# Optimization experiments

Measured on AMD Instinct MI355X. Metric: run time of the kernel, lower is better.

Reference implementation:

```python
import jax, jax.numpy as jnp
import numpy as np

N, E, G = 50000, 800000, 64        # nodes, edges, graphs in batch
IN, HID, OUT = 64, 128, 8


def gcn_conv(x, W, b, src, dst, num_nodes):
    """GCNConv: h = D^-1/2 (A+I) D^-1/2 (x W) + b, self-loops already in src/dst."""
    h = x @ W                                              # [N, out]
    deg = jax.ops.segment_sum(jnp.ones_like(dst, dtype=h.dtype), dst,
                              num_segments=num_nodes)      # [N]
    dinv = jax.lax.rsqrt(jnp.maximum(deg, 1.0))
    norm = dinv[src] * dinv[dst]                           # [E+N]
    msg = h[src] * norm[:, None]                           # gather + scale
    out = jax.ops.segment_sum(msg, dst, num_segments=num_nodes)
    return out + b


def global_mean_pool(x, batch, num_graphs):
    s = jax.ops.segment_sum(x, batch, num_segments=num_graphs)
    cnt = jax.ops.segment_sum(jnp.ones((x.shape[0],), x.dtype), batch,
                              num_segments=num_graphs)
    return s / jnp.maximum(cnt, 1.0)[:, None]


def setup_inputs() -> dict:
    key = jax.random.key(0)
    ks = jax.random.split(key, 11)
    def glorot(k, fi, fo):
        return jax.random.normal(k, (fi, fo), jnp.float32) * np.float32(1.0 / np.sqrt(fi))
    return {
        "x": jax.random.normal(ks[0], (N, IN), jnp.float32),
        "W1": glorot(ks[1], IN, HID),  "b1": jnp.zeros((HID,), jnp.float32),
        "W2": glorot(ks[2], HID, HID), "b2": jnp.zeros((HID,), jnp.float32),
        "W3": glorot(ks[3], HID, HID), "b3": jnp.zeros((HID,), jnp.float32),
        "Wh": glorot(ks[4], HID, OUT), "bh": jnp.zeros((OUT,), jnp.float32),
        "edge_index": jax.random.randint(ks[5], (2, E), 0, N),
        "batch": jnp.sort(jax.random.randint(ks[6], (N,), 0, G)),
    }


def reference(x, W1, b1, W2, b2, W3, b3, Wh, bh, edge_index, batch):
    loops = jnp.arange(N, dtype=edge_index.dtype)
    src = jnp.concatenate([edge_index[0], loops])          # add self-loops
    dst = jnp.concatenate([edge_index[1], loops])
    h = jax.nn.relu(gcn_conv(x, W1, b1, src, dst, N))
    h = jax.nn.relu(gcn_conv(h, W2, b2, src, dst, N))
    h = gcn_conv(h, W3, b3, src, dst, N)
    g = global_mean_pool(h, batch, G)                      # [G, HID]
    return g @ Wh + bh                                     # [G, OUT]
```

## Files before the change

### kernel.cpp

```cpp
#include <hip/hip_runtime.h>

typedef short bf8_t __attribute__((ext_vector_type(8)));
typedef float f32x4 __attribute__((ext_vector_type(4)));
typedef unsigned short u16;

__device__ inline u16 f2bf(float f) {
    unsigned u = __float_as_uint(f);
    return (u16)((u + 0x7fff + ((u >> 16) & 1)) >> 16);
}


__global__ void deg_kernel(const int* __restrict__ dst, int* __restrict__ deg,
                           u16* __restrict__ rank, int E) {
    int e = blockIdx.x * 256 + threadIdx.x;
    if (e < E) rank[e] = (u16)atomicAdd(&deg[dst[e]], 1);
}

__global__ void scan_blocksum(const int* __restrict__ deg, int* __restrict__ bsum,
                              float* __restrict__ dinv, int n) {
    int i = blockIdx.x * 256 + threadIdx.x;
    int d = (i < n) ? (deg[i] + 1) : 0;
    if (i < n) dinv[i] = rsqrtf((float)d);
    int v = d;
    for (int off = 32; off > 0; off >>= 1) v += __shfl_down(v, off, 64);
    __shared__ int ws[4];
    if ((threadIdx.x & 63) == 0) ws[threadIdx.x >> 6] = v;
    __syncthreads();
    if (threadIdx.x == 0) bsum[blockIdx.x] = ws[0] + ws[1] + ws[2] + ws[3];
}

__global__ void scan_offsets(const int* __restrict__ bsum, int* __restrict__ boff, int nblk) {
    __shared__ int buf[256];
    int tid = threadIdx.x;
    int v = (tid < nblk) ? bsum[tid] : 0;
    buf[tid] = v;
    __syncthreads();
    for (int off = 1; off < 256; off <<= 1) {
        int t = (tid >= off) ? buf[tid - off] : 0;
        __syncthreads();
        buf[tid] += t;
        __syncthreads();
    }
    if (tid < nblk) boff[tid] = buf[tid] - v;
}

__global__ void scan_rowptr(const int* __restrict__ deg, const int* __restrict__ boff,
                            int* __restrict__ row_ptr, int n) {
    __shared__ int buf[256];
    int tid = threadIdx.x;
    int i = blockIdx.x * 256 + tid;
    int v = (i < n) ? (deg[i] + 1) : 0;
    buf[tid] = v;
    __syncthreads();
    for (int off = 1; off < 256; off <<= 1) {
        int t = (tid >= off) ? buf[tid - off] : 0;
        __syncthreads();
        buf[tid] += t;
        __syncthreads();
    }
    int excl = buf[tid] - v + boff[blockIdx.x];
    if (i < n) row_ptr[i] = excl;
    if (i == n - 1) row_ptr[n] = excl + v;
}

__global__ void fill_kernel(const int* __restrict__ src, const int* __restrict__ dst,
                            const u16* __restrict__ rank,
                            const int* __restrict__ row_ptr,
                            u16* __restrict__ csr_src, int E, int n) {
    int e = blockIdx.x * 256 + threadIdx.x;
    if (e < E) {
        int s = src[e], d = dst[e];
        int pos = row_ptr[d] + 1 + (int)rank[e];
        __builtin_nontemporal_store((u16)s, &csr_src[pos]);
    } else if (e < E + n) {
        int s = e - E;
        __builtin_nontemporal_store((u16)s, &csr_src[row_ptr[s]]);
    }
}

__global__ void x2bf_kernel(const float* __restrict__ x, const float* __restrict__ dinv,
                            unsigned* __restrict__ x16, int total8) {
    int i = blockIdx.x * 256 + threadIdx.x;
    if (i >= total8) return;
    float dn = dinv[i >> 3];
    const float4* x4 = (const float4*)x;
    float4 a = x4[i * 2], b = x4[i * 2 + 1];
    uint4 o;
    o.x = (unsigned)f2bf(a.x * dn) | ((unsigned)f2bf(a.y * dn) << 16);
    o.y = (unsigned)f2bf(a.z * dn) | ((unsigned)f2bf(a.w * dn) << 16);
    o.z = (unsigned)f2bf(b.x * dn) | ((unsigned)f2bf(b.y * dn) << 16);
    o.w = (unsigned)f2bf(b.z * dn) | ((unsigned)f2bf(b.w * dn) << 16);
    ((uint4*)x16)[i] = o;
}

__global__ void wt_all(const float* __restrict__ W1, const float* __restrict__ W2,
                       const float* __restrict__ W3,
                       u16* __restrict__ Wt1, u16* __restrict__ Wt2,
                       u16* __restrict__ Wt3) {
    int i = blockIdx.x * 256 + threadIdx.x;
    if (i < 8192) {
        int nn = i / 64, k = i - nn * 64;
        Wt1[i] = f2bf(W1[k * 128 + nn]);
    } else if (i < 24576) {
        int j = i - 8192;
        int nn = j / 128, k = j - nn * 128;
        Wt2[j] = f2bf(W2[k * 128 + nn]);
    } else if (i < 40960) {
        int j = i - 24576;
        int nn = j / 128, k = j - nn * 128;
        Wt3[j] = f2bf(W3[k * 128 + nn]);
    }
}


__device__ inline void bf8_add(uint4 a, float* acc) {
#pragma unroll
    for (int j = 0; j < 4; ++j) {
        unsigned u = ((const unsigned*)&a)[j];
        acc[2 * j]     += __uint_as_float(u << 16);
        acc[2 * j + 1] += __uint_as_float(u & 0xffff0000u);
    }
}

__device__ inline uint4 pack_bf8(const float* v, float dn) {
    uint4 o;
    o.x = (unsigned)f2bf(v[0] * dn) | ((unsigned)f2bf(v[1] * dn) << 16);
    o.y = (unsigned)f2bf(v[2] * dn) | ((unsigned)f2bf(v[3] * dn) << 16);
    o.z = (unsigned)f2bf(v[4] * dn) | ((unsigned)f2bf(v[5] * dn) << 16);
    o.w = (unsigned)f2bf(v[6] * dn) | ((unsigned)f2bf(v[7] * dn) << 16);
    return o;
}

template<int K, bool RELU, bool BF16OUT>
__global__ __launch_bounds__(256) void agg_gemm(
        const u16* __restrict__ in, const u16* __restrict__ Wt16,
        const float* __restrict__ bias, void* __restrict__ outp,
        const int* __restrict__ row_ptr, const u16* __restrict__ csr_src,
        const float* __restrict__ dinv, int n) {
    constexpr int KS = K / 32;
    __shared__ u16 As[16 * K];
    int w = threadIdx.x >> 6, lane = threadIdx.x & 63;
    int base = blockIdx.x * 16;
    int lr = lane & 15, lk = lane >> 4;

    bf8_t B[2][KS];
#pragma unroll
    for (int f = 0; f < 2; ++f) {
        int col = w * 32 + f * 16 + lr;
#pragma unroll
        for (int ks = 0; ks < KS; ++ks)
            B[f][ks] = *reinterpret_cast<const bf8_t*>(&Wt16[(size_t)col * K + ks * 32 + lk * 8]);
    }

    const uint4* in4 = (const uint4*)in;
    int g = lane >> 4;
    int row = w * 4 + g;
    int node = base + row;
    float acc[8] = {0.f, 0.f, 0.f, 0.f, 0.f, 0.f, 0.f, 0.f};

    if (K == 128) {
        int col = lane & 15;
        if (node < n) {
            int beg = row_ptr[node], end = row_ptr[node + 1];
            int i = beg;
            int s0 = csr_src[i], s1 = csr_src[i + 1];
            for (; i + 1 < end; i += 2) {
                int t0 = csr_src[i + 2], t1 = csr_src[i + 3];
                uint4 a = in4[(size_t)s0 * 16 + col];
                uint4 b = in4[(size_t)s1 * 16 + col];
                bf8_add(a, acc);
                bf8_add(b, acc);
                s0 = t0; s1 = t1;
            }
            if (i < end) bf8_add(in4[(size_t)s0 * 16 + col], acc);
        }
        float dn = (node < n) ? dinv[node] : 0.f;
        int off = row * K + ((col * 8) ^ ((row & 7) << 3));
        *(uint4*)&As[off] = pack_bf8(acc, dn);
    } else {
        int sub = (lane >> 3) & 1;
        int col = lane & 7;
        if (node < n) {
            int beg = row_ptr[node], end = row_ptr[node + 1];
            int i = beg + sub;
            int s0 = csr_src[i], s1 = csr_src[i + 2];
            for (; i + 2 < end; i += 4) {
                int t0 = csr_src[i + 4], t1 = csr_src[i + 6];
                uint4 a = in4[(size_t)s0 * 8 + col];
                uint4 b = in4[(size_t)s1 * 8 + col];
                bf8_add(a, acc);
                bf8_add(b, acc);
                s0 = t0; s1 = t1;
            }
            if (i < end) bf8_add(in4[(size_t)s0 * 8 + col], acc);
        }
#pragma unroll
        for (int j = 0; j < 8; ++j)
            acc[j] += __shfl_xor(acc[j], 8, 64);
        if (sub == 0) {
            float dn = (node < n) ? dinv[node] : 0.f;
            int off = row * K + ((col * 8) ^ ((row & 7) << 3));
            *(uint4*)&As[off] = pack_bf8(acc, dn);
        }
    }
    __syncthreads();

    f32x4 pacc[2] = {};
#pragma unroll
    for (int ks = 0; ks < KS; ++ks) {
        int off = lr * K + (((ks * 32) + lk * 8) ^ ((lr & 7) << 3));
        bf8_t a = *reinterpret_cast<const bf8_t*>(&As[off]);
#pragma unroll
        for (int f = 0; f < 2; ++f)
            pacc[f] = __builtin_amdgcn_mfma_f32_16x16x32_bf16(B[f][ks], a, pacc[f], 0, 0, 0);
    }

    int orow = base + lr;
    if (orow < n) {
        float dnx = BF16OUT ? dinv[orow] : 1.f;
#pragma unroll
        for (int f = 0; f < 2; ++f) {
            int c0 = w * 32 + f * 16 + lk * 4;
            float4 bv = *(const float4*)&bias[c0];
            float v0 = pacc[f][0] + bv.x, v1 = pacc[f][1] + bv.y;
            float v2 = pacc[f][2] + bv.z, v3 = pacc[f][3] + bv.w;
            if (RELU) {
                v0 = fmaxf(v0, 0.f); v1 = fmaxf(v1, 0.f);
                v2 = fmaxf(v2, 0.f); v3 = fmaxf(v3, 0.f);
            }
            if (BF16OUT) {
                uint2 o;
                o.x = (unsigned)f2bf(v0 * dnx) | ((unsigned)f2bf(v1 * dnx) << 16);
                o.y = (unsigned)f2bf(v2 * dnx) | ((unsigned)f2bf(v3 * dnx) << 16);
                *(uint2*)&((u16*)outp)[(size_t)orow * 128 + c0] = o;
            } else {
                *(float4*)&((float*)outp)[(size_t)orow * 128 + c0] = make_float4(v0, v1, v2, v3);
            }
        }
    }
}


__device__ inline int lbound(const int* __restrict__ batch, int n, int g) {
    int lo = 0, hi = n;
    while (lo < hi) {
        int mid = (lo + hi) >> 1;
        if (batch[mid] < g) lo = mid + 1; else hi = mid;
    }
    return lo;
}

#define PSPLIT 16
__global__ __launch_bounds__(256) void pool_part(
        const float* __restrict__ h, const int* __restrict__ batch,
        float* __restrict__ part, int n) {
    int g = blockIdx.x >> 4, sp = blockIdx.x & (PSPLIT - 1);
    int tid = threadIdx.x;
    int c = tid & 127, rs = tid >> 7;
    int beg = lbound(batch, n, g), end = lbound(batch, n, g + 1);
    int len = end - beg;
    int chunk = (len + PSPLIT - 1) >> 4;
    int r0 = beg + sp * chunk;
    int r1 = min(r0 + chunk, end);
    float acc = 0.f;
    for (int r = r0 + rs; r < r1; r += 2)
        acc += h[(size_t)r * 128 + c];
    __shared__ float buf[256];
    buf[tid] = acc;
    __syncthreads();
    if (rs == 0)
        part[(size_t)blockIdx.x * 128 + c] = buf[c] + buf[c + 128];
}

__global__ __launch_bounds__(128) void pool_final(
        const float* __restrict__ part, const int* __restrict__ batch,
        float* __restrict__ gout, int n) {
    int g = blockIdx.x;
    int c = threadIdx.x;
    float acc = 0.f;
#pragma unroll
    for (int sp = 0; sp < PSPLIT; ++sp)
        acc += part[((size_t)g * PSPLIT + sp) * 128 + c];
    int cnt = lbound(batch, n, g + 1) - lbound(batch, n, g);
    gout[g * 128 + c] = acc / fmaxf((float)cnt, 1.f);
}

__global__ void head_kernel(const float* __restrict__ g, const float* __restrict__ Wh,
                            const float* __restrict__ bh, float* __restrict__ out, int G) {
    int tid = blockIdx.x * blockDim.x + threadIdx.x;
    if (tid >= G * 8) return;
    int gi = tid >> 3, o = tid & 7;
    float acc = bh[o];
    for (int k = 0; k < 128; ++k)
        acc = fmaf(g[gi * 128 + k], Wh[k * 8 + o], acc);
    out[tid] = acc;
}


extern "C" void kernel_launch(void* const* d_in, const int* in_sizes, int n_in,
                              void* d_out, int out_size, void* d_ws, size_t ws_size,
                              hipStream_t stream) {
    const float* x  = (const float*)d_in[0];
    const float* W1 = (const float*)d_in[1];
    const float* b1 = (const float*)d_in[2];
    const float* W2 = (const float*)d_in[3];
    const float* b2 = (const float*)d_in[4];
    const float* W3 = (const float*)d_in[5];
    const float* b3 = (const float*)d_in[6];
    const float* Wh = (const float*)d_in[7];
    const float* bh = (const float*)d_in[8];
    const int* edge_index = (const int*)d_in[9];
    const int* batch = (const int*)d_in[10];
    (void)n_in; (void)ws_size;

    const int N = in_sizes[10];
    const int E = in_sizes[9] / 2;
    const int G = out_size / 8;
    const int* esrc = edge_index;
    const int* edst = edge_index + E;

    size_t off = 0;
    auto take = [&](size_t bytes) {
        void* p = (char*)d_ws + off;
        off += (bytes + 255) & ~(size_t)255;
        return p;
    };
    int*   deg      = (int*)take((size_t)N * 4);
    float* dinv     = (float*)take((size_t)N * 4);
    int*   row_ptr  = (int*)take((size_t)(N + 1) * 4);
    u16*   rank     = (u16*)take((size_t)E * 2);
    u16*   csr_src  = (u16*)take((size_t)(E + N + 64) * 2);
    int*   bsum     = (int*)take(256 * 4);
    int*   boff     = (int*)take(256 * 4);
    float* part     = (float*)take((size_t)G * PSPLIT * 128 * 4);
    float* gpool    = (float*)take((size_t)G * 128 * 4);
    u16*   x16      = (u16*)take((size_t)N * 64 * 2);
    u16*   h16a     = (u16*)take((size_t)N * 128 * 2);
    u16*   h16b     = (u16*)take((size_t)N * 128 * 2);
    u16*   Wt1      = (u16*)take((size_t)128 * 64 * 2);
    u16*   Wt2      = (u16*)take((size_t)128 * 128 * 2);
    u16*   Wt3      = (u16*)take((size_t)128 * 128 * 2);
    float* bufA     = (float*)take((size_t)N * 128 * 4);

    int nblk = (N + 255) / 256;
    int fgrid = (N + 15) / 16;

    hipMemsetAsync(deg, 0, (size_t)N * 4, stream);

    deg_kernel<<<(E + 255) / 256, 256, 0, stream>>>(edst, deg, rank, E);
    scan_blocksum<<<nblk, 256, 0, stream>>>(deg, bsum, dinv, N);
    scan_offsets<<<1, 256, 0, stream>>>(bsum, boff, nblk);
    scan_rowptr<<<nblk, 256, 0, stream>>>(deg, boff, row_ptr, N);
    fill_kernel<<<(E + N + 255) / 256, 256, 0, stream>>>(esrc, edst, rank, row_ptr, csr_src, E, N);
    x2bf_kernel<<<(N * 64 / 8 + 255) / 256, 256, 0, stream>>>(x, dinv, (unsigned*)x16, N * 64 / 8);
    wt_all<<<(40960 + 255) / 256, 256, 0, stream>>>(W1, W2, W3, Wt1, Wt2, Wt3);

    agg_gemm<64,  true,  true ><<<fgrid, 256, 0, stream>>>(x16,  Wt1, b1, h16a, row_ptr, csr_src, dinv, N);
    agg_gemm<128, true,  true ><<<fgrid, 256, 0, stream>>>(h16a, Wt2, b2, h16b, row_ptr, csr_src, dinv, N);
    agg_gemm<128, false, false><<<fgrid, 256, 0, stream>>>(h16b, Wt3, b3, bufA, row_ptr, csr_src, dinv, N);

    pool_part<<<G * PSPLIT, 256, 0, stream>>>(bufA, batch, part, N);
    pool_final<<<G, 128, 0, stream>>>(part, batch, gpool, N);
    head_kernel<<<(G * 8 + 255) / 256, 256, 0, stream>>>(gpool, Wh, bh, (float*)d_out, G);
}
```

Baseline: 224.5 us.

## Fuse prep kernels and pooling head; use nontemporal gather loads

Merges the CSR fill, x-to-bf16 conversion and weight transpose kernels into one prep launch, and folds the head matmul into the pool-final kernel, so there are fewer kernel launches and gaps between them. The neighbour-feature gathers in the aggregation kernels now use nontemporal loads through a vector type. The intent is to cut launch overhead and to reduce cache pollution from the random gathers. The risk is that nontemporal hints hurt reuse, because feature rows are gathered many times and could otherwise be served from L2.

```diff
diff --git a/kernel.cpp b/kernel.cpp
--- a/kernel.cpp
+++ b/kernel.cpp
@@ -2,6 +2,7 @@
 
 typedef short bf8_t __attribute__((ext_vector_type(8)));
 typedef float f32x4 __attribute__((ext_vector_type(4)));
+typedef unsigned u32x4 __attribute__((ext_vector_type(4)));
 typedef unsigned short u16;
 
 __device__ inline u16 f2bf(float f) {
@@ -63,71 +64,73 @@
     if (i == n - 1) row_ptr[n] = excl + v;
 }
 
-__global__ void fill_kernel(const int* __restrict__ src, const int* __restrict__ dst,
-                            const u16* __restrict__ rank,
-                            const int* __restrict__ row_ptr,
-                            u16* __restrict__ csr_src, int E, int n) {
-    int e = blockIdx.x * 256 + threadIdx.x;
-    if (e < E) {
-        int s = src[e], d = dst[e];
-        int pos = row_ptr[d] + 1 + (int)rank[e];
+
+__global__ void prep_kernel(const int* __restrict__ src, const int* __restrict__ dst,
+                            const u16* __restrict__ rank, const int* __restrict__ row_ptr,
+                            u16* __restrict__ csr_src,
+                            const float* __restrict__ x, const float* __restrict__ dinv,
+                            unsigned* __restrict__ x16,
+                            const float* __restrict__ W1, const float* __restrict__ W2,
+                            const float* __restrict__ W3,
+                            u16* __restrict__ Wt1, u16* __restrict__ Wt2,
+                            u16* __restrict__ Wt3,
+                            int E, int n, int total8) {
+    int gid = blockIdx.x * 256 + threadIdx.x;
+    if (gid < E) {
+        int s = src[gid], d = dst[gid];
+        int pos = row_ptr[d] + 1 + (int)rank[gid];
         __builtin_nontemporal_store((u16)s, &csr_src[pos]);
-    } else if (e < E + n) {
-        int s = e - E;
+        return;
+    }
+    if (gid < E + n) {
+        int s = gid - E;
         __builtin_nontemporal_store((u16)s, &csr_src[row_ptr[s]]);
-    }
-}
-
-__global__ void x2bf_kernel(const float* __restrict__ x, const float* __restrict__ dinv,
-                            unsigned* __restrict__ x16, int total8) {
-    int i = blockIdx.x * 256 + threadIdx.x;
-    if (i >= total8) return;
-    float dn = dinv[i >> 3];
-    const float4* x4 = (const float4*)x;
-    float4 a = x4[i * 2], b = x4[i * 2 + 1];
-    uint4 o;
-    o.x = (unsigned)f2bf(a.x * dn) | ((unsigned)f2bf(a.y * dn) << 16);
-    o.y = (unsigned)f2bf(a.z * dn) | ((unsigned)f2bf(a.w * dn) << 16);
-    o.z = (unsigned)f2bf(b.x * dn) | ((unsigned)f2bf(b.y * dn) << 16);
-    o.w = (unsigned)f2bf(b.z * dn) | ((unsigned)f2bf(b.w * dn) << 16);
-    ((uint4*)x16)[i] = o;
-}
-
-__global__ void wt_all(const float* __restrict__ W1, const float* __restrict__ W2,
-                       const float* __restrict__ W3,
-                       u16* __restrict__ Wt1, u16* __restrict__ Wt2,
-                       u16* __restrict__ Wt3) {
-    int i = blockIdx.x * 256 + threadIdx.x;
-    if (i < 8192) {
-        int nn = i / 64, k = i - nn * 64;
-        Wt1[i] = f2bf(W1[k * 128 + nn]);
-    } else if (i < 24576) {
-        int j = i - 8192;
-        int nn = j / 128, k = j - nn * 128;
-        Wt2[j] = f2bf(W2[k * 128 + nn]);
-    } else if (i < 40960) {
-        int j = i - 24576;
-        int nn = j / 128, k = j - nn * 128;
-        Wt3[j] = f2bf(W3[k * 128 + nn]);
-    }
-}
-
-
-__device__ inline void bf8_add(uint4 a, float* acc) {
+        return;
+    }
+    int i = gid - (E + n);
+    if (i < total8) {
+        float dn = dinv[i >> 3];
+        const float4* x4 = (const float4*)x;
+        float4 a = x4[i * 2], b = x4[i * 2 + 1];
+        uint4 o;
+        o.x = (unsigned)f2bf(a.x * dn) | ((unsigned)f2bf(a.y * dn) << 16);
+        o.y = (unsigned)f2bf(a.z * dn) | ((unsigned)f2bf(a.w * dn) << 16);
+        o.z = (unsigned)f2bf(b.x * dn) | ((unsigned)f2bf(b.y * dn) << 16);
+        o.w = (unsigned)f2bf(b.z * dn) | ((unsigned)f2bf(b.w * dn) << 16);
+        ((uint4*)x16)[i] = o;
+        return;
+    }
+    int j = i - total8;
+    if (j < 8192) {
+        int nn = j / 64, k = j - nn * 64;
+        Wt1[j] = f2bf(W1[k * 128 + nn]);
+    } else if (j < 24576) {
+        int jj = j - 8192;
+        int nn = jj / 128, k = jj - nn * 128;
+        Wt2[jj] = f2bf(W2[k * 128 + nn]);
+    } else if (j < 40960) {
+        int jj = j - 24576;
+        int nn = jj / 128, k = jj - nn * 128;
+        Wt3[jj] = f2bf(W3[k * 128 + nn]);
+    }
+}
+
+
+__device__ inline void bf8_add(u32x4 a, float* acc) {
 #pragma unroll
     for (int j = 0; j < 4; ++j) {
-        unsigned u = ((const unsigned*)&a)[j];
+        unsigned u = a[j];
         acc[2 * j]     += __uint_as_float(u << 16);
         acc[2 * j + 1] += __uint_as_float(u & 0xffff0000u);
     }
 }
 
-__device__ inline uint4 pack_bf8(const float* v, float dn) {
-    uint4 o;
-    o.x = (unsigned)f2bf(v[0] * dn) | ((unsigned)f2bf(v[1] * dn) << 16);
-    o.y = (unsigned)f2bf(v[2] * dn) | ((unsigned)f2bf(v[3] * dn) << 16);
-    o.z = (unsigned)f2bf(v[4] * dn) | ((unsigned)f2bf(v[5] * dn) << 16);
-    o.w = (unsigned)f2bf(v[6] * dn) | ((unsigned)f2bf(v[7] * dn) << 16);
+__device__ inline u32x4 pack_bf8(const float* v, float dn) {
+    u32x4 o;
+    o[0] = (unsigned)f2bf(v[0] * dn) | ((unsigned)f2bf(v[1] * dn) << 16);
+    o[1] = (unsigned)f2bf(v[2] * dn) | ((unsigned)f2bf(v[3] * dn) << 16);
+    o[2] = (unsigned)f2bf(v[4] * dn) | ((unsigned)f2bf(v[5] * dn) << 16);
+    o[3] = (unsigned)f2bf(v[6] * dn) | ((unsigned)f2bf(v[7] * dn) << 16);
     return o;
 }
 
@@ -152,7 +155,7 @@
             B[f][ks] = *reinterpret_cast<const bf8_t*>(&Wt16[(size_t)col * K + ks * 32 + lk * 8]);
     }
 
-    const uint4* in4 = (const uint4*)in;
+    const u32x4* in4 = (const u32x4*)in;
     int g = lane >> 4;
     int row = w * 4 + g;
     int node = base + row;
@@ -166,17 +169,17 @@
             int s0 = csr_src[i], s1 = csr_src[i + 1];
             for (; i + 1 < end; i += 2) {
                 int t0 = csr_src[i + 2], t1 = csr_src[i + 3];
-                uint4 a = in4[(size_t)s0 * 16 + col];
-                uint4 b = in4[(size_t)s1 * 16 + col];
+                u32x4 a = __builtin_nontemporal_load(&in4[(size_t)s0 * 16 + col]);
+                u32x4 b = __builtin_nontemporal_load(&in4[(size_t)s1 * 16 + col]);
                 bf8_add(a, acc);
                 bf8_add(b, acc);
                 s0 = t0; s1 = t1;
             }
-            if (i < end) bf8_add(in4[(size_t)s0 * 16 + col], acc);
+            if (i < end) bf8_add(__builtin_nontemporal_load(&in4[(size_t)s0 * 16 + col]), acc);
         }
         float dn = (node < n) ? dinv[node] : 0.f;
         int off = row * K + ((col * 8) ^ ((row & 7) << 3));
-        *(uint4*)&As[off] = pack_bf8(acc, dn);
+        *(u32x4*)&As[off] = pack_bf8(acc, dn);
     } else {
         int sub = (lane >> 3) & 1;
         int col = lane & 7;
@@ -186,13 +189,13 @@
             int s0 = csr_src[i], s1 = csr_src[i + 2];
             for (; i + 2 < end; i += 4) {
                 int t0 = csr_src[i + 4], t1 = csr_src[i + 6];
-                uint4 a = in4[(size_t)s0 * 8 + col];
-                uint4 b = in4[(size_t)s1 * 8 + col];
+                u32x4 a = __builtin_nontemporal_load(&in4[(size_t)s0 * 8 + col]);
+                u32x4 b = __builtin_nontemporal_load(&in4[(size_t)s1 * 8 + col]);
                 bf8_add(a, acc);
                 bf8_add(b, acc);
                 s0 = t0; s1 = t1;
             }
-            if (i < end) bf8_add(in4[(size_t)s0 * 8 + col], acc);
+            if (i < end) bf8_add(__builtin_nontemporal_load(&in4[(size_t)s0 * 8 + col]), acc);
         }
 #pragma unroll
         for (int j = 0; j < 8; ++j)
@@ -200,7 +203,7 @@
         if (sub == 0) {
             float dn = (node < n) ? dinv[node] : 0.f;
             int off = row * K + ((col * 8) ^ ((row & 7) << 3));
-            *(uint4*)&As[off] = pack_bf8(acc, dn);
+            *(u32x4*)&As[off] = pack_bf8(acc, dn);
         }
     }
     __syncthreads();
@@ -272,28 +275,32 @@
         part[(size_t)blockIdx.x * 128 + c] = buf[c] + buf[c + 128];
 }
 
-__global__ __launch_bounds__(128) void pool_final(
+__global__ __launch_bounds__(128) void pool_head(
         const float* __restrict__ part, const int* __restrict__ batch,
-        float* __restrict__ gout, int n) {
+        const float* __restrict__ Wh, const float* __restrict__ bh,
+        float* __restrict__ out, int n) {
     int g = blockIdx.x;
-    int c = threadIdx.x;
+    int tid = threadIdx.x;
     float acc = 0.f;
 #pragma unroll
     for (int sp = 0; sp < PSPLIT; ++sp)
-        acc += part[((size_t)g * PSPLIT + sp) * 128 + c];
+        acc += part[((size_t)g * PSPLIT + sp) * 128 + tid];
     int cnt = lbound(batch, n, g + 1) - lbound(batch, n, g);
-    gout[g * 128 + c] = acc / fmaxf((float)cnt, 1.f);
-}
-
-__global__ void head_kernel(const float* __restrict__ g, const float* __restrict__ Wh,
-                            const float* __restrict__ bh, float* __restrict__ out, int G) {
-    int tid = blockIdx.x * blockDim.x + threadIdx.x;
-    if (tid >= G * 8) return;
-    int gi = tid >> 3, o = tid & 7;
-    float acc = bh[o];
-    for (int k = 0; k < 128; ++k)
-        acc = fmaf(g[gi * 128 + k], Wh[k * 8 + o], acc);
-    out[tid] = acc;
+    __shared__ float grow[128];
+    grow[tid] = acc / fmaxf((float)cnt, 1.f);
+    __syncthreads();
+    int sub = tid >> 3, o = tid & 7;
+    float p = 0.f;
+    for (int k = sub; k < 128; k += 16)
+        p += grow[k] * Wh[k * 8 + o];
+    __shared__ float p2[128];
+    p2[tid] = p;
+    __syncthreads();
+    for (int s = 8; s > 0; s >>= 1) {
+        if (sub < s) p2[sub * 8 + o] += p2[(sub + s) * 8 + o];
+        __syncthreads();
+    }
+    if (tid < 8) out[g * 8 + tid] = p2[tid] + bh[tid];
 }
 
 
@@ -333,7 +340,6 @@
     int*   bsum     = (int*)take(256 * 4);
     int*   boff     = (int*)take(256 * 4);
     float* part     = (float*)take((size_t)G * PSPLIT * 128 * 4);
-    float* gpool    = (float*)take((size_t)G * 128 * 4);
     u16*   x16      = (u16*)take((size_t)N * 64 * 2);
     u16*   h16a     = (u16*)take((size_t)N * 128 * 2);
     u16*   h16b     = (u16*)take((size_t)N * 128 * 2);
@@ -342,8 +348,10 @@
     u16*   Wt3      = (u16*)take((size_t)128 * 128 * 2);
     float* bufA     = (float*)take((size_t)N * 128 * 4);
 
-    int nblk = (N + 255) / 256;
+    int nblk  = (N + 255) / 256;
     int fgrid = (N + 15) / 16;
+    int total8 = N * 64 / 8;
+    int prep_threads = E + N + total8 + 40960;
 
     hipMemsetAsync(deg, 0, (size_t)N * 4, stream);
 
@@ -351,15 +359,14 @@
     scan_blocksum<<<nblk, 256, 0, stream>>>(deg, bsum, dinv, N);
     scan_offsets<<<1, 256, 0, stream>>>(bsum, boff, nblk);
     scan_rowptr<<<nblk, 256, 0, stream>>>(deg, boff, row_ptr, N);
-    fill_kernel<<<(E + N + 255) / 256, 256, 0, stream>>>(esrc, edst, rank, row_ptr, csr_src, E, N);
-    x2bf_kernel<<<(N * 64 / 8 + 255) / 256, 256, 0, stream>>>(x, dinv, (unsigned*)x16, N * 64 / 8);
-    wt_all<<<(40960 + 255) / 256, 256, 0, stream>>>(W1, W2, W3, Wt1, Wt2, Wt3);
+    prep_kernel<<<(prep_threads + 255) / 256, 256, 0, stream>>>(
+        esrc, edst, rank, row_ptr, csr_src, x, dinv, (unsigned*)x16,
+        W1, W2, W3, Wt1, Wt2, Wt3, E, N, total8);
 
     agg_gemm<64,  true,  true ><<<fgrid, 256, 0, stream>>>(x16,  Wt1, b1, h16a, row_ptr, csr_src, dinv, N);
     agg_gemm<128, true,  true ><<<fgrid, 256, 0, stream>>>(h16a, Wt2, b2, h16b, row_ptr, csr_src, dinv, N);
     agg_gemm<128, false, false><<<fgrid, 256, 0, stream>>>(h16b, Wt3, b3, bufA, row_ptr, csr_src, dinv, N);
 
     pool_part<<<G * PSPLIT, 256, 0, stream>>>(bufA, batch, part, N);
-    pool_final<<<G, 128, 0, stream>>>(part, batch, gpool, N);
-    head_kernel<<<(G * 8 + 255) / 256, 256, 0, stream>>>(gpool, Wh, bh, (float*)d_out, G);
-}
+    pool_head<<<G, 128, 0, stream>>>(part, batch, Wh, bh, (float*)d_out, N);
+}
```

Measured after the change: 256.4 us. 14.2% more time.
